# Kernel tuning notes

Hardware: AMD Instinct MI355X
Metric: run time of the kernel (lower is better)

The kernel has to match this reference:

```python
import jax, jax.numpy as jnp
import numpy as np

# module hyper-parameters (from init_kwargs)
IN_H, IN_W = 64, 44
OUT_H, OUT_W = 48, 22
DT_OFF, DX_OFF, DY_OFF = 0.5, 0.5, 0.5
SIGMA_OFF, DELTA_OFF = 1.0, 1.0
EPS = 1e-8
K_PO = 2  # ProgressiveOffset k


def _progressive_offset(v, k=K_PO):
    # torch: x += detach(x) shifted right by i with zero fill, scaled 1/k, for i=1..k
    vd = jax.lax.stop_gradient(v)
    out = v
    T = v.shape[1]
    for i in range(1, k + 1):
        out = out + jnp.pad(vd, ((0, 0), (i, 0)))[:, :T] * (1.0 / k)
    return out


def setup_inputs() -> dict:
    key = jax.random.key(0)
    ks = jax.random.split(key, 9)
    N, C, T = 16, 64, 30
    return {
        "x": jax.random.normal(ks[0], (N, C, T, IN_H, IN_W), jnp.float32),
        "dx": jax.random.normal(ks[1], (N, T), jnp.float32),
        "dy": jax.random.normal(ks[2], (N, T), jnp.float32),
        "log_sigma2": jax.random.normal(ks[3], (N, T), jnp.float32),
        "log_delta": jax.random.normal(ks[4], (N, T), jnp.float32),
        "log_gamma": jax.random.normal(ks[5], (N, T), jnp.float32),
        "dt": jax.random.normal(ks[6], (N,), jnp.float32),
        "log_delta_t": jax.random.normal(ks[7], (N,), jnp.float32),
        "log_gamma_t": jax.random.normal(ks[8], (N,), jnp.float32),
    }


def reference(x, dx, dy, log_sigma2, log_delta, log_gamma, dt, log_delta_t, log_gamma_t):
    N, C, T, H, W = x.shape
    NT = N * T
    a_w = OUT_W
    a_h = int(round(OUT_W / IN_W * IN_H))  # attended spatial height (32)

    anchor_t = T * DT_OFF
    anchor_x = W * DX_OFF
    anchor_y = H * DY_OFF

    # --- localization params ---
    dxv = jnp.tanh(_progressive_offset(dx).reshape(NT, 1)) * (IN_W / 2.0) + anchor_x
    dyv = jnp.tanh(_progressive_offset(dy).reshape(NT, 1)) * (IN_H / 2.0) + anchor_y
    sigma2 = jnp.exp(log_sigma2).reshape(NT, 1) * SIGMA_OFF
    delta = jnp.exp(log_delta).reshape(NT, 1) * DELTA_OFF
    gamma = jax.nn.sigmoid(log_gamma).reshape(NT)
    dtv = jnp.tanh(dt) * (T / 2.0) + anchor_t           # (N,)
    delta_t = jnp.exp(log_delta_t) * DELTA_OFF          # (N,)
    gamma_t = jax.nn.sigmoid(log_gamma_t)               # (N,)

    # --- Gaussian spatial filter banks ---
    gx = jnp.arange(a_w, dtype=x.dtype)
    gy = jnp.arange(a_h, dtype=x.dtype)
    mu_x = dxv + (gx[None, :] - a_w / 2.0) * delta      # (NT, a_w)
    mu_y = dyv + (gy[None, :] - a_h / 2.0) * delta      # (NT, a_h)
    a = jnp.arange(W, dtype=x.dtype)[None, None, :]
    b = jnp.arange(H, dtype=x.dtype)[None, None, :]
    s2 = sigma2[:, :, None]                              # (NT,1,1)
    Fx = jnp.exp(-((a - mu_x[:, :, None]) ** 2) / (2.0 * s2))  # (NT, a_w, W)
    Fy = jnp.exp(-((b - mu_y[:, :, None]) ** 2) / (2.0 * s2))  # (NT, a_h, H)
    Fx = Fx / jnp.maximum(jnp.sum(Fx, axis=2, keepdims=True), EPS)
    Fy = Fy / jnp.maximum(jnp.sum(Fy, axis=2, keepdims=True), EPS)

    # --- spatial glimpse: Fy @ x @ Fx^T, batched over (N*T, C) ---
    xf = jnp.transpose(x, (0, 2, 1, 3, 4)).reshape(NT, C, H, W)
    glimpse = jnp.einsum('nih,nchw,njw->ncij', Fy, xf, Fx)  # (NT, C, a_h, a_w)
    glimpse = glimpse * gamma[:, None, None, None]

    # --- temporal transform (grid_sample, align_corners=False, zero padding) ---
    gt = jnp.arange(T, dtype=x.dtype)
    mu_t = dtv[:, None] + (gt[None, :] - T / 2.0) * delta_t[:, None]  # (N, T)
    mu_t = mu_t / (T - 1) * 2.0 - 1.0
    # y-axis sample coords in input index space
    iy = ((mu_t + 1.0) * T - 1.0) / 2.0
    iy0 = jnp.floor(iy)
    w1 = iy - iy0
    w0 = 1.0 - w1
    i0 = iy0.astype(jnp.int32)
    i1 = i0 + 1
    v0 = ((i0 >= 0) & (i0 < T)).astype(x.dtype)
    v1 = ((i1 >= 0) & (i1 < T)).astype(x.dtype)
    g = glimpse.reshape(N, T, C * a_h * a_w)             # (N, T, Chw)
    g0 = jnp.take_along_axis(g, jnp.clip(i0, 0, T - 1)[:, :, None], axis=1)
    g1 = jnp.take_along_axis(g, jnp.clip(i1, 0, T - 1)[:, :, None], axis=1)
    # x-grid coord is fixed at -1 with width-1 input -> factor 0.5 (half in zero pad)
    out_t = 0.5 * ((w0 * v0)[:, :, None] * g0 + (w1 * v1)[:, :, None] * g1)

    out = out_t.reshape(N, T, C, a_h, a_w).transpose(0, 2, 1, 3, 4)  # (N,C,T,a_h,a_w)
    out = out * gamma_t[:, None, None, None, None]

    pad_t = (OUT_H - a_h) // 2
    pad_b = OUT_H - pad_t - a_h
    out = jnp.pad(out, ((0, 0), (0, 0), (0, 0), (pad_t, pad_b), (0, 0)))
    return out
```

## Files before the change

### kernel.cpp

```cpp
#include <hip/hip_runtime.h>
#include <math.h>


#define EPS_ 1e-8f

__global__ __launch_bounds__(256) void gst_kernel(
    const float* __restrict__ x,
    const float* __restrict__ dx,  const float* __restrict__ dy,
    const float* __restrict__ ls2, const float* __restrict__ ld,
    const float* __restrict__ lg,
    const float* __restrict__ dtp, const float* __restrict__ ldt,
    const float* __restrict__ lgt,
    float* __restrict__ out)
{
    __shared__ float FyT[64][32];
    __shared__ float FxT[44][24];
    __shared__ float t2s[8][32][26];

    const int tid = threadIdx.x;
    int b = blockIdx.x;
    const int cg = b & 7; b >>= 3;
    const int tq = b % 30;
    const int n  = b / 30;

    const float dtv     = tanhf(dtp[n]) * 15.f + 15.f;
    const float delta_t = expf(ldt[n]);
    const float gamma_t = 1.f / (1.f + expf(-lgt[n]));
    float mu_t = dtv + ((float)tq - 15.f) * delta_t;
    mu_t = mu_t / 29.f * 2.f - 1.f;
    const float iy  = ((mu_t + 1.f) * 30.f - 1.f) * 0.5f;
    const float iy0 = floorf(iy);
    const float w1  = iy - iy0;
    const int   i0  = (int)iy0;
    const int   i1  = i0 + 1;
    const float W0 = (i0 >= 0 && i0 < 30) ? 0.5f * gamma_t * (1.f - w1) : 0.f;
    const float W1 = (i1 >= 0 && i1 < 30) ? 0.5f * gamma_t * w1 : 0.f;
    const int t0 = min(max(i0, 0), 29);
    const int t1 = min(max(i1, 0), 29);

    const int c_loc = tid >> 5;
    const int jt    = tid & 3;
    const int it    = (tid >> 2) & 7;
    const int j0    = 6 * jt;
    const int i0r   = 4 * it;

    const int c1 = tid >> 4;
    const int hl = tid & 15;

    float acc2[4][6];
#pragma unroll
    for (int r = 0; r < 4; ++r)
#pragma unroll
        for (int s2 = 0; s2 < 6; ++s2) acc2[r][s2] = 0.f;

    bool first = true;
#pragma unroll 1
    for (int s = 0; s < 2; ++s) {
        const float Ws = s ? W1 : W0;
        const int   ts = s ? t1 : t0;
        if (Ws == 0.f) continue;
        if (!first) __syncthreads();
        first = false;

        const int nt = n * 30 + ts;
        const float sigma2 = expf(ls2[nt]);
        const float inv2s2 = 0.5f / sigma2;
        const float delta  = expf(ld[nt]);
        const float gamma  = 1.f / (1.f + expf(-lg[nt]));
        const float A      = Ws * gamma;

        if (tid < 128) {
            const int i = tid >> 2, q = tid & 3;
            float pod = dy[nt] + 0.5f * (ts >= 1 ? dy[nt - 1] : 0.f)
                               + 0.5f * (ts >= 2 ? dy[nt - 2] : 0.f);
            const float mu = tanhf(pod) * 32.f + 32.f + ((float)i - 16.f) * delta;
            float e[16];
            float sum = 0.f;
#pragma unroll
            for (int k = 0; k < 16; ++k) {
                const float d = (float)(16 * q + k) - mu;
                e[k] = expf(-d * d * inv2s2);
                sum += e[k];
            }
            sum += __shfl_xor(sum, 1);
            sum += __shfl_xor(sum, 2);
            const float sc = A / fmaxf(sum, EPS_);
#pragma unroll
            for (int k = 0; k < 16; ++k)
                FyT[16 * q + k][i] = e[k] * sc;
        } else {
            const int tx = tid - 128;
            const int j = tx >> 2, q = tx & 3;
            float pod = dx[nt] + 0.5f * (ts >= 1 ? dx[nt - 1] : 0.f)
                               + 0.5f * (ts >= 2 ? dx[nt - 2] : 0.f);
            const float mu = tanhf(pod) * 22.f + 22.f + ((float)j - 11.f) * delta;
            float e[11];
            float sum = 0.f;
#pragma unroll
            for (int m = 0; m < 11; ++m) {
                const float d = (float)(11 * q + m) - mu;
                e[m] = expf(-d * d * inv2s2);
                sum += e[m];
            }
            sum += __shfl_xor(sum, 1);
            sum += __shfl_xor(sum, 2);
            const float sc = 1.f / fmaxf(sum, EPS_);
            if (j < 22) {
#pragma unroll
                for (int m = 0; m < 11; ++m)
                    FxT[11 * q + m][j] = e[m] * sc;
            }
        }
        __syncthreads();

#pragma unroll 1
        for (int hc = 0; hc < 2; ++hc) {
            if (tid < 128) {
                float a0[22], a1[22];
#pragma unroll
                for (int j = 0; j < 22; ++j) { a0[j] = 0.f; a1[j] = 0.f; }

                const size_t xoff =
                    ((((size_t)n * 64 + (size_t)(cg * 8 + c1)) * 30
                      + (size_t)ts) * 64 + (size_t)(32 * hc + hl)) * 44;
                const float4* xr0 = reinterpret_cast<const float4*>(x + xoff);
                const float4* xr1 = reinterpret_cast<const float4*>(x + xoff + 16 * 44);

#pragma unroll 2
                for (int wi = 0; wi < 11; ++wi) {
                    const float4 xa = xr0[wi];
                    const float4 xb = xr1[wi];
                    const float xav[4] = { xa.x, xa.y, xa.z, xa.w };
                    const float xbv[4] = { xb.x, xb.y, xb.z, xb.w };
#pragma unroll
                    for (int k = 0; k < 4; ++k) {
                        const float4* fxr =
                            reinterpret_cast<const float4*>(&FxT[4 * wi + k][0]);
                        const float4 f0 = fxr[0], f1 = fxr[1], f2 = fxr[2],
                                     f3 = fxr[3], f4 = fxr[4];
                        const float2 f5 =
                            *reinterpret_cast<const float2*>(&FxT[4 * wi + k][20]);
                        const float fv[22] = { f0.x, f0.y, f0.z, f0.w,
                                               f1.x, f1.y, f1.z, f1.w,
                                               f2.x, f2.y, f2.z, f2.w,
                                               f3.x, f3.y, f3.z, f3.w,
                                               f4.x, f4.y, f4.z, f4.w,
                                               f5.x, f5.y };
                        const float va = xav[k], vb = xbv[k];
#pragma unroll
                        for (int j = 0; j < 22; ++j) {
                            a0[j] += va * fv[j];
                            a1[j] += vb * fv[j];
                        }
                    }
                }
                float2* d0 = reinterpret_cast<float2*>(&t2s[c1][hl][0]);
                float2* d1 = reinterpret_cast<float2*>(&t2s[c1][hl + 16][0]);
#pragma unroll
                for (int p = 0; p < 11; ++p) {
                    d0[p] = make_float2(a0[2 * p], a0[2 * p + 1]);
                    d1[p] = make_float2(a1[2 * p], a1[2 * p + 1]);
                }
                d0[11] = make_float2(0.f, 0.f);
                d1[11] = make_float2(0.f, 0.f);
            }
            __syncthreads();

            {
#pragma unroll 4
                for (int hp2 = 0; hp2 < 32; ++hp2) {
                    const float4 fy =
                        *reinterpret_cast<const float4*>(&FyT[32 * hc + hp2][i0r]);
                    const float2* tp =
                        reinterpret_cast<const float2*>(&t2s[c_loc][hp2][j0]);
                    const float2 q0 = tp[0], q1 = tp[1], q2 = tp[2];
                    const float fyv[4] = { fy.x, fy.y, fy.z, fy.w };
                    const float tv[6]  = { q0.x, q0.y, q1.x, q1.y, q2.x, q2.y };
#pragma unroll
                    for (int r = 0; r < 4; ++r)
#pragma unroll
                        for (int s2 = 0; s2 < 6; ++s2)
                            acc2[r][s2] += fyv[r] * tv[s2];
                }
            }
            if (hc == 0) __syncthreads();
        }
    }

    const size_t ob =
        (((size_t)n * 64 + (size_t)(cg * 8)) * 30 + (size_t)tq) * 1056;

    for (int idx = tid; idx < 8 * 16 * 22; idx += 256) {
        const int c   = idx / 352;
        const int rem = idx % 352;
        const int r   = rem / 22;
        const int j   = rem % 22;
        const int ip  = (r < 8) ? r : (r + 32);
        out[ob + (size_t)c * 31680 + (size_t)(ip * 22 + j)] = 0.f;
    }

#pragma unroll
    for (int r = 0; r < 4; ++r) {
#pragma unroll
        for (int s2 = 0; s2 < 6; ++s2) {
            const int j = j0 + s2;
            if (j < 22) {
                out[ob + (size_t)c_loc * 31680
                       + (size_t)((8 + i0r + r) * 22 + j)] = acc2[r][s2];
            }
        }
    }
}

extern "C" void kernel_launch(void* const* d_in, const int* in_sizes, int n_in,
                              void* d_out, int out_size, void* d_ws, size_t ws_size,
                              hipStream_t stream) {
    const float* x   = (const float*)d_in[0];
    const float* dx  = (const float*)d_in[1];
    const float* dy  = (const float*)d_in[2];
    const float* ls2 = (const float*)d_in[3];
    const float* ld  = (const float*)d_in[4];
    const float* lg  = (const float*)d_in[5];
    const float* dtp = (const float*)d_in[6];
    const float* ldt = (const float*)d_in[7];
    const float* lgt = (const float*)d_in[8];
    float* out = (float*)d_out;

    dim3 grid(16 * 30 * 8), block(256);
    hipLaunchKernelGGL(gst_kernel, grid, block, 0, stream,
                       x, dx, dy, ls2, ld, lg, dtp, ldt, lgt, out);
}
```

Measured before the change: 643.9 us.

## Use all 256 threads for the W-contraction and hoist padding-zero stores

The first (W) contraction now runs on all 256 threads instead of 128. Each thread handles one channel and one row pair (h, h+32), covering all 64 input rows in one pass rather than two hc passes. Partial results are staged to shared memory in two halves, each followed by an H-contraction, which removes the idle half-block during the x loads and FMA work. The zero-fill of the padding rows moves to kernel start so those stores overlap with compute. The trade-off is more live registers per thread (a0/a1 held across syncs) and an extra barrier per slice.

New measurement: 624.6 us. -3.0%, faster.

```diff
diff --git a/kernel.cpp b/kernel.cpp
--- a/kernel.cpp
+++ b/kernel.cpp
@@ -39,13 +39,22 @@
     const int t1 = min(max(i1, 0), 29);
 
     const int c_loc = tid >> 5;
+    const int hl    = tid & 31;
     const int jt    = tid & 3;
     const int it    = (tid >> 2) & 7;
     const int j0    = 6 * jt;
     const int i0r   = 4 * it;
 
-    const int c1 = tid >> 4;
-    const int hl = tid & 15;
+    const size_t ob =
+        (((size_t)n * 64 + (size_t)(cg * 8)) * 30 + (size_t)tq) * 1056;
+    for (int idx = tid; idx < 8 * 16 * 22; idx += 256) {
+        const int c   = idx / 352;
+        const int rem = idx % 352;
+        const int r   = rem / 22;
+        const int j   = rem % 22;
+        const int ip  = (r < 8) ? r : (r + 32);
+        out[ob + (size_t)c * 31680 + (size_t)(ip * 22 + j)] = 0.f;
+    }
 
     float acc2[4][6];
 #pragma unroll
@@ -110,93 +119,105 @@
                 for (int m = 0; m < 11; ++m)
                     FxT[11 * q + m][j] = e[m] * sc;
             }
-        }
-        __syncthreads();
-
-#pragma unroll 1
-        for (int hc = 0; hc < 2; ++hc) {
-            if (tid < 128) {
-                float a0[22], a1[22];
-#pragma unroll
-                for (int j = 0; j < 22; ++j) { a0[j] = 0.f; a1[j] = 0.f; }
-
-                const size_t xoff =
-                    ((((size_t)n * 64 + (size_t)(cg * 8 + c1)) * 30
-                      + (size_t)ts) * 64 + (size_t)(32 * hc + hl)) * 44;
-                const float4* xr0 = reinterpret_cast<const float4*>(x + xoff);
-                const float4* xr1 = reinterpret_cast<const float4*>(x + xoff + 16 * 44);
+            if (j < 22 && q == 3) {  }
+        }
+        if (tid < 88) {
+            FxT[tid >> 1][22 + (tid & 1)] = 0.f;
+        }
+        __syncthreads();
+
+        float a0[22], a1[22];
+#pragma unroll
+        for (int j = 0; j < 22; ++j) { a0[j] = 0.f; a1[j] = 0.f; }
+        {
+            const size_t xoff =
+                ((((size_t)n * 64 + (size_t)(cg * 8 + c_loc)) * 30
+                  + (size_t)ts) * 64 + (size_t)hl) * 44;
+            const float4* xr0 = reinterpret_cast<const float4*>(x + xoff);
+            const float4* xr1 = reinterpret_cast<const float4*>(x + xoff + 32 * 44);
 
 #pragma unroll 2
-                for (int wi = 0; wi < 11; ++wi) {
-                    const float4 xa = xr0[wi];
-                    const float4 xb = xr1[wi];
-                    const float xav[4] = { xa.x, xa.y, xa.z, xa.w };
-                    const float xbv[4] = { xb.x, xb.y, xb.z, xb.w };
-#pragma unroll
-                    for (int k = 0; k < 4; ++k) {
-                        const float4* fxr =
-                            reinterpret_cast<const float4*>(&FxT[4 * wi + k][0]);
-                        const float4 f0 = fxr[0], f1 = fxr[1], f2 = fxr[2],
-                                     f3 = fxr[3], f4 = fxr[4];
-                        const float2 f5 =
-                            *reinterpret_cast<const float2*>(&FxT[4 * wi + k][20]);
-                        const float fv[22] = { f0.x, f0.y, f0.z, f0.w,
-                                               f1.x, f1.y, f1.z, f1.w,
-                                               f2.x, f2.y, f2.z, f2.w,
-                                               f3.x, f3.y, f3.z, f3.w,
-                                               f4.x, f4.y, f4.z, f4.w,
-                                               f5.x, f5.y };
-                        const float va = xav[k], vb = xbv[k];
-#pragma unroll
-                        for (int j = 0; j < 22; ++j) {
-                            a0[j] += va * fv[j];
-                            a1[j] += vb * fv[j];
-                        }
+            for (int wi = 0; wi < 11; ++wi) {
+                const float4 xa = xr0[wi];
+                const float4 xb = xr1[wi];
+                const float xav[4] = { xa.x, xa.y, xa.z, xa.w };
+                const float xbv[4] = { xb.x, xb.y, xb.z, xb.w };
+#pragma unroll
+                for (int k = 0; k < 4; ++k) {
+                    const float4* fxr =
+                        reinterpret_cast<const float4*>(&FxT[4 * wi + k][0]);
+                    const float4 f0 = fxr[0], f1 = fxr[1], f2 = fxr[2],
+                                 f3 = fxr[3], f4 = fxr[4];
+                    const float2 f5 =
+                        *reinterpret_cast<const float2*>(&FxT[4 * wi + k][20]);
+                    const float fv[22] = { f0.x, f0.y, f0.z, f0.w,
+                                           f1.x, f1.y, f1.z, f1.w,
+                                           f2.x, f2.y, f2.z, f2.w,
+                                           f3.x, f3.y, f3.z, f3.w,
+                                           f4.x, f4.y, f4.z, f4.w,
+                                           f5.x, f5.y };
+                    const float va = xav[k], vb = xbv[k];
+#pragma unroll
+                    for (int j = 0; j < 22; ++j) {
+                        a0[j] += va * fv[j];
+                        a1[j] += vb * fv[j];
                     }
                 }
-                float2* d0 = reinterpret_cast<float2*>(&t2s[c1][hl][0]);
-                float2* d1 = reinterpret_cast<float2*>(&t2s[c1][hl + 16][0]);
-#pragma unroll
-                for (int p = 0; p < 11; ++p) {
-                    d0[p] = make_float2(a0[2 * p], a0[2 * p + 1]);
-                    d1[p] = make_float2(a1[2 * p], a1[2 * p + 1]);
-                }
-                d0[11] = make_float2(0.f, 0.f);
-                d1[11] = make_float2(0.f, 0.f);
-            }
-            __syncthreads();
-
-            {
+            }
+        }
+
+        {
+            float2* d0 = reinterpret_cast<float2*>(&t2s[c_loc][hl][0]);
+#pragma unroll
+            for (int p = 0; p < 11; ++p)
+                d0[p] = make_float2(a0[2 * p], a0[2 * p + 1]);
+            d0[11] = make_float2(0.f, 0.f);
+        }
+        __syncthreads();
+        {
 #pragma unroll 4
-                for (int hp2 = 0; hp2 < 32; ++hp2) {
-                    const float4 fy =
-                        *reinterpret_cast<const float4*>(&FyT[32 * hc + hp2][i0r]);
-                    const float2* tp =
-                        reinterpret_cast<const float2*>(&t2s[c_loc][hp2][j0]);
-                    const float2 q0 = tp[0], q1 = tp[1], q2 = tp[2];
-                    const float fyv[4] = { fy.x, fy.y, fy.z, fy.w };
-                    const float tv[6]  = { q0.x, q0.y, q1.x, q1.y, q2.x, q2.y };
-#pragma unroll
-                    for (int r = 0; r < 4; ++r)
-#pragma unroll
-                        for (int s2 = 0; s2 < 6; ++s2)
-                            acc2[r][s2] += fyv[r] * tv[s2];
-                }
-            }
-            if (hc == 0) __syncthreads();
-        }
-    }
-
-    const size_t ob =
-        (((size_t)n * 64 + (size_t)(cg * 8)) * 30 + (size_t)tq) * 1056;
-
-    for (int idx = tid; idx < 8 * 16 * 22; idx += 256) {
-        const int c   = idx / 352;
-        const int rem = idx % 352;
-        const int r   = rem / 22;
-        const int j   = rem % 22;
-        const int ip  = (r < 8) ? r : (r + 32);
-        out[ob + (size_t)c * 31680 + (size_t)(ip * 22 + j)] = 0.f;
+            for (int hp2 = 0; hp2 < 32; ++hp2) {
+                const float4 fy =
+                    *reinterpret_cast<const float4*>(&FyT[hp2][i0r]);
+                const float2* tp =
+                    reinterpret_cast<const float2*>(&t2s[c_loc][hp2][j0]);
+                const float2 q0 = tp[0], q1 = tp[1], q2 = tp[2];
+                const float fyv[4] = { fy.x, fy.y, fy.z, fy.w };
+                const float tv[6]  = { q0.x, q0.y, q1.x, q1.y, q2.x, q2.y };
+#pragma unroll
+                for (int r = 0; r < 4; ++r)
+#pragma unroll
+                    for (int s2 = 0; s2 < 6; ++s2)
+                        acc2[r][s2] += fyv[r] * tv[s2];
+            }
+        }
+        __syncthreads();
+
+        {
+            float2* d1 = reinterpret_cast<float2*>(&t2s[c_loc][hl][0]);
+#pragma unroll
+            for (int p = 0; p < 11; ++p)
+                d1[p] = make_float2(a1[2 * p], a1[2 * p + 1]);
+            d1[11] = make_float2(0.f, 0.f);
+        }
+        __syncthreads();
+        {
+#pragma unroll 4
+            for (int hp2 = 0; hp2 < 32; ++hp2) {
+                const float4 fy =
+                    *reinterpret_cast<const float4*>(&FyT[32 + hp2][i0r]);
+                const float2* tp =
+                    reinterpret_cast<const float2*>(&t2s[c_loc][hp2][j0]);
+                const float2 q0 = tp[0], q1 = tp[1], q2 = tp[2];
+                const float fyv[4] = { fy.x, fy.y, fy.z, fy.w };
+                const float tv[6]  = { q0.x, q0.y, q1.x, q1.y, q2.x, q2.y };
+#pragma unroll
+                for (int r = 0; r < 4; ++r)
+#pragma unroll
+                    for (int s2 = 0; s2 < 6; ++s2)
+                        acc2[r][s2] += fyv[r] * tv[s2];
+            }
+        }
     }
 
 #pragma unroll
```
